# Kernel optimization log

Hardware: AMD Instinct MI355X
Metric: run time of the kernel (lower is better)

The kernel has to match this reference:

```python
import jax, jax.numpy as jnp
import numpy as np

TAU = 1.0
K_ROUTE = 3
EPS = 1e-8


def setup_inputs() -> dict:
    key = jax.random.key(0)
    ks = jax.random.split(key, 8)
    B, T, D_in, H, D_out, L, d_addr = 8, 8192, 1024, 1024, 1024, 12, 64

    def unit_rows(k, L_, d_):
        U = jax.random.normal(k, (L_, d_), dtype=jnp.float32)
        U = U - U.mean(axis=1, keepdims=True)
        return U / (jnp.linalg.norm(U, axis=1, keepdims=True) + EPS)

    def norm_tape(k, shape):
        W = jax.random.normal(k, shape, dtype=jnp.float32)
        # F.normalize over last two dims per expert
        n = jnp.sqrt(jnp.sum(W * W, axis=tuple(range(1, W.ndim)), keepdims=True)) + 1e-12
        return W / n

    x = jax.random.normal(ks[0], (B, T, D_in), dtype=jnp.float32)
    P_w = jax.random.normal(ks[1], (d_addr, D_in), dtype=jnp.float32) / np.sqrt(D_in)
    U1 = unit_rows(ks[2], L, d_addr)
    U2 = unit_rows(ks[3], L, d_addr)
    U3 = unit_rows(ks[4], L, d_addr)
    W1 = norm_tape(ks[5], (L, H, D_in))
    W2 = norm_tape(ks[6], (L, D_out, H))
    b2 = norm_tape(ks[7], (L, D_out))
    return {"x": x, "P_w": P_w, "U1": U1, "U2": U2, "U3": U3,
            "W1": W1, "W2": W2, "b2": b2}


def _route_combine_weights(x_addr, U, k, tau):
    """Top-k routing -> dense combine matrix C: [N, L], zero off the top-k.
    Mathematically identical to scattering softmax(topv/tau) onto expert slots,
    matching RouterTopK.forward + the grouped dispatch/combine."""
    z = x_addr @ U.T                      # [N, L]
    topv, topi = jax.lax.top_k(z, k)      # [N, k]
    w = jax.nn.softmax(topv / (tau + EPS), axis=1)
    N, L = z.shape
    rows = jnp.arange(N)[:, None]
    return jnp.zeros((N, L), z.dtype).at[rows, topi].add(w)


def _mixture(inp, C, W):
    """y[n] = sum_e C[n,e] * (W[e] @ inp[n]); C is top-k sparse per row.
    Loop over the small fixed expert count L (12) with one dense GEMM each;
    equals _apply_mixture_grouped since C is zero for unselected experts."""
    L = W.shape[0]
    y = jnp.zeros((inp.shape[0], W.shape[1]), inp.dtype)
    for e in range(L):
        y = y + C[:, e:e + 1] * (inp @ W[e].T)
    return y


def reference(x, P_w, U1, U2, U3, W1, W2, b2):
    B, T, D = x.shape
    xf = x.reshape(B * T, D)              # [N, D_in]
    xa = xf @ P_w.T                       # [N, d_addr]
    C1 = _route_combine_weights(xa, U1, K_ROUTE, TAU)
    C2 = _route_combine_weights(xa, U2, K_ROUTE, TAU)
    C3 = _route_combine_weights(xa, U3, K_ROUTE, TAU)
    h = jax.nn.gelu(_mixture(xf, C1, W1), approximate=False)  # nn.GELU (exact)
    y = _mixture(h, C2, W2) + C3 @ b2      # routed bias == _apply_bias_grouped
    return y.reshape(B, T, -1)
```

## Files before the change

### kernel.cpp

```cpp
#include <hip/hip_runtime.h>

#define NTOT 65536

typedef __attribute__((ext_vector_type(8))) short bf16x8;
typedef __attribute__((ext_vector_type(4))) float f32x4;

__device__ __forceinline__ float bf2f(unsigned short u) {
    union { unsigned int i; float f; } v; v.i = ((unsigned int)u) << 16; return v.f;
}
__device__ __forceinline__ unsigned short f2bf(float f) {
    union { float f; unsigned int i; } v; v.f = f;
    unsigned int i = v.i;
    return (unsigned short)((i + 0x7FFFu + ((i >> 16) & 1u)) >> 16);
}
__device__ __forceinline__ float lo16(unsigned int v) { return bf2f((unsigned short)(v & 0xFFFFu)); }
__device__ __forceinline__ float hi16(unsigned int v) { return bf2f((unsigned short)(v >> 16)); }

__device__ __forceinline__ void gload16(const unsigned short* g, unsigned short* l) {
    __builtin_amdgcn_global_load_lds((const __attribute__((address_space(1))) void*)(g),
                                     (__attribute__((address_space(3))) void*)(l), 16, 0, 0);
}

__global__ __launch_bounds__(256) void cvt_bf16(const float* __restrict__ src,
                                                unsigned short* __restrict__ dst) {
    size_t i = ((size_t)blockIdx.x * 256 + threadIdx.x) * 8;
    float4 a = *(const float4*)(src + i);
    float4 b = *(const float4*)(src + i + 4);
    unsigned int o0 = (unsigned int)f2bf(a.x) | ((unsigned int)f2bf(a.y) << 16);
    unsigned int o1 = (unsigned int)f2bf(a.z) | ((unsigned int)f2bf(a.w) << 16);
    unsigned int o2 = (unsigned int)f2bf(b.x) | ((unsigned int)f2bf(b.y) << 16);
    unsigned int o3 = (unsigned int)f2bf(b.z) | ((unsigned int)f2bf(b.w) << 16);
    uint4 o = {o0, o1, o2, o3};
    *(uint4*)(dst + i) = o;
}

__global__ void zero_counts(int* c1, int* c2) {
    if (threadIdx.x < 16) { c1[threadIdx.x] = 0; c2[threadIdx.x] = 0; }
}

__global__ __launch_bounds__(256, 2) void addr_xa(const float* __restrict__ X,
                                                  const float* __restrict__ Pw,
                                                  double* __restrict__ xa, int tok_base) {
    __shared__ float xs[64 * 133];
    __shared__ float ps[64 * 133];
    const int tid = threadIdx.x;
    const int tb = blockIdx.x * 64;
    const int ta = tid & 15, tt = tid >> 4;
    double acc[4][4];
    for (int i = 0; i < 4; i++) for (int j = 0; j < 4; j++) acc[i][j] = 0.0;
    for (int kc = 0; kc < 8; ++kc) {
        int k0 = kc * 128;
        for (int i = 0; i < 8; ++i) {
            int lin = i * 256 + tid;
            int row = lin >> 5;
            int c4 = lin & 31;
            float4 v = *(const float4*)&X[(size_t)(tok_base + tb + row) * 1024 + k0 + c4 * 4];
            *(float4*)&xs[row * 133 + c4 * 4] = v;
            float4 w = *(const float4*)&Pw[(size_t)row * 1024 + k0 + c4 * 4];
            *(float4*)&ps[row * 133 + c4 * 4] = w;
        }
        __syncthreads();
        for (int k = 0; k < 128; k += 4) {
            float4 xv[4], pv[4];
            for (int i = 0; i < 4; ++i) xv[i] = *(const float4*)&xs[(tt * 4 + i) * 133 + k];
            for (int j = 0; j < 4; ++j) pv[j] = *(const float4*)&ps[(ta * 4 + j) * 133 + k];
            for (int i = 0; i < 4; ++i)
                for (int j = 0; j < 4; ++j) {
                    double s = acc[i][j];
                    s += (double)xv[i].x * (double)pv[j].x;
                    s += (double)xv[i].y * (double)pv[j].y;
                    s += (double)xv[i].z * (double)pv[j].z;
                    s += (double)xv[i].w * (double)pv[j].w;
                    acc[i][j] = s;
                }
        }
        __syncthreads();
    }
    for (int i = 0; i < 4; ++i)
        for (int j = 0; j < 4; ++j)
            xa[(size_t)(tb + tt * 4 + i) * 64 + ta * 4 + j] = acc[i][j];
}

__global__ __launch_bounds__(256) void route_kernel(
    const double* __restrict__ xa,
    const float* __restrict__ U1, const float* __restrict__ U2, const float* __restrict__ U3,
    int* __restrict__ counts1, int* __restrict__ counts2,
    int* __restrict__ bucket1, float* __restrict__ bucketw1,
    int* __restrict__ bucket2, float* __restrict__ bucketw2,
    int* __restrict__ topi3, float* __restrict__ topw3, int Nc) {
    __shared__ float Us[3 * 12 * 64];
    __shared__ int lcnt1[12], lcnt2[12], gbase1[12], gbase2[12];
    int tid = threadIdx.x;
    for (int i = tid; i < 3 * 12 * 64; i += 256) {
        int l = i / (12 * 64), rem = i % (12 * 64);
        const float* Up = (l == 0 ? U1 : (l == 1 ? U2 : U3));
        Us[i] = Up[rem];
    }
    if (tid < 12) { lcnt1[tid] = 0; lcnt2[tid] = 0; }
    __syncthreads();
    int n = blockIdx.x * 256 + tid;
    double xv[64];
    for (int a = 0; a < 64; a += 2) {
        double2 v = *(const double2*)&xa[(size_t)n * 64 + a];
        xv[a] = v.x; xv[a + 1] = v.y;
    }
    int ei[3][3]; float ew[3][3];
    for (int l = 0; l < 3; l++) {
        double z[12];
        for (int e = 0; e < 12; e++) {
            double s = 0.0;
            const float* u = &Us[(l * 12 + e) * 64];
            for (int a = 0; a < 64; a++) s += xv[a] * (double)u[a];
            z[e] = s;
        }
        int i0 = 0, i1 = 0, i2 = 0; double v0 = -1e300, v1 = -1e300, v2 = -1e300;
        for (int e = 0; e < 12; e++) {
            double v = z[e];
            if (v > v0)      { v2 = v1; i2 = i1; v1 = v0; i1 = i0; v0 = v; i0 = e; }
            else if (v > v1) { v2 = v1; i2 = i1; v1 = v; i1 = e; }
            else if (v > v2) { v2 = v; i2 = e; }
        }
        float inv = 1.0f / (1.0f + 1e-8f);
        float e1 = expf((float)(v1 - v0) * inv), e2 = expf((float)(v2 - v0) * inv);
        float s = 1.0f + e1 + e2;
        ew[l][0] = 1.0f / s; ew[l][1] = e1 / s; ew[l][2] = e2 / s;
        ei[l][0] = i0; ei[l][1] = i1; ei[l][2] = i2;
    }
    int lpos1[3], lpos2[3];
    for (int s = 0; s < 3; s++) {
        lpos1[s] = atomicAdd(&lcnt1[ei[0][s]], 1);
        lpos2[s] = atomicAdd(&lcnt2[ei[1][s]], 1);
    }
    __syncthreads();
    if (tid < 12) {
        gbase1[tid] = atomicAdd(&counts1[tid], lcnt1[tid]);
        gbase2[tid] = atomicAdd(&counts2[tid], lcnt2[tid]);
    }
    __syncthreads();
    for (int s = 0; s < 3; s++) {
        int e = ei[0][s]; int pos = gbase1[e] + lpos1[s];
        bucket1[e * Nc + pos] = (s << 16) | n;
        bucketw1[e * Nc + pos] = ew[0][s];
        e = ei[1][s]; pos = gbase2[e] + lpos2[s];
        bucket2[e * Nc + pos] = (s << 16) | n;
        bucketw2[e * Nc + pos] = ew[1][s];
        topi3[n * 3 + s] = ei[2][s];
        topw3[n * 3 + s] = ew[2][s];
    }
}

__global__ __launch_bounds__(256) void grouped_gemm(
    const unsigned short* __restrict__ A,
    const unsigned short* __restrict__ W,
    const int* __restrict__ bucket, const float* __restrict__ bucketw,
    const int* __restrict__ counts,
    unsigned short* __restrict__ part, int Nc) {
    __shared__ unsigned short As[128 * 32];
    __shared__ unsigned short Bs[128 * 32];
    __shared__ int ids[128];
    __shared__ float wts[128];
    int bx = blockIdx.x;
    int e = -1, mt = 0, accum = 0, Me = 0;
    for (int ee = 0; ee < 12; ee++) {
        int c = counts[ee];
        int t = (c + 127) >> 7;
        if (e < 0 && bx < accum + t) { e = ee; mt = bx - accum; Me = c; }
        accum += t;
    }
    if (e < 0) return;
    int nt = blockIdx.y;
    int tid = threadIdx.x, lane = tid & 63, w = tid >> 6;
    int m0 = mt << 7;
    if (tid < 128) {
        int r = m0 + tid; if (r >= Me) r = Me - 1;
        ids[tid] = bucket[e * Nc + r];
        wts[tid] = bucketw[e * Nc + r];
    }
    __syncthreads();
    int seg = lane & 3;
    int rA0 = w * 16 + (lane >> 2);
    int rA1 = rA0 + 64;
    const unsigned short* a0p = A + (size_t)(ids[rA0] & 0xFFFF) * 1024 + seg * 8;
    const unsigned short* a1p = A + (size_t)(ids[rA1] & 0xFFFF) * 1024 + seg * 8;
    const unsigned short* b0p = W + (size_t)e * 1048576 + (size_t)(nt * 128 + rA0) * 1024 + seg * 8;
    const unsigned short* b1p = W + (size_t)e * 1048576 + (size_t)(nt * 128 + rA1) * 1024 + seg * 8;
    unsigned short* AsL0 = &As[w * 512 + lane * 8];
    unsigned short* AsL1 = &As[(w + 4) * 512 + lane * 8];
    unsigned short* BsL0 = &Bs[w * 512 + lane * 8];
    unsigned short* BsL1 = &Bs[(w + 4) * 512 + lane * 8];
    f32x4 acc[4][4];
    for (int i = 0; i < 4; i++) for (int j = 0; j < 4; j++) acc[i][j] = (f32x4){0.f, 0.f, 0.f, 0.f};
    int wr0 = (w & 1) * 64, wc0 = (w >> 1) * 64;
    for (int it = 0; it < 32; ++it) {
        int k0 = it * 32;
        gload16(a0p + k0, AsL0);
        gload16(a1p + k0, AsL1);
        gload16(b0p + k0, BsL0);
        gload16(b1p + k0, BsL1);
        __syncthreads();
        int q = lane >> 4, l15 = lane & 15;
        bf16x8 af[4], bfr[4];
        for (int i = 0; i < 4; i++) af[i]  = *(const bf16x8*)&As[(wr0 + i * 16 + l15) * 32 + q * 8];
        for (int j = 0; j < 4; j++) bfr[j] = *(const bf16x8*)&Bs[(wc0 + j * 16 + l15) * 32 + q * 8];
        for (int i = 0; i < 4; i++)
            for (int j = 0; j < 4; j++)
                acc[i][j] = __builtin_amdgcn_mfma_f32_16x16x32_bf16(af[i], bfr[j], acc[i][j], 0, 0, 0);
        __syncthreads();
    }
    int q = lane >> 4, l15 = lane & 15;
    for (int i = 0; i < 4; i++) {
        for (int r = 0; r < 4; r++) {
            int row = wr0 + i * 16 + q * 4 + r;
            if (m0 + row >= Me) continue;
            int id = ids[row];
            int n = id & 0xFFFF, slot = id >> 16;
            float wt = wts[row];
            size_t base = ((size_t)slot * Nc + n) * 1024 + (size_t)(nt * 128 + wc0);
            for (int j = 0; j < 4; j++)
                part[base + j * 16 + l15] = f2bf(acc[i][j][r] * wt);
        }
    }
}

__global__ __launch_bounds__(256) void combine_gelu(const unsigned short* __restrict__ part,
                                                    unsigned short* __restrict__ h, int Nc) {
    size_t idx = ((size_t)blockIdx.x * 256 + threadIdx.x) * 8;
    const size_t S = (size_t)Nc * 1024;
    uint4 a = *(const uint4*)(part + idx);
    uint4 b = *(const uint4*)(part + S + idx);
    uint4 c = *(const uint4*)(part + 2 * S + idx);
    unsigned int pa[4] = {a.x, a.y, a.z, a.w};
    unsigned int pb[4] = {b.x, b.y, b.z, b.w};
    unsigned int pc[4] = {c.x, c.y, c.z, c.w};
    unsigned int po[4];
    for (int k = 0; k < 4; k++) {
        float s0 = lo16(pa[k]) + lo16(pb[k]) + lo16(pc[k]);
        float s1 = hi16(pa[k]) + hi16(pb[k]) + hi16(pc[k]);
        float g0 = 0.5f * s0 * (1.0f + erff(s0 * 0.70710678118654752f));
        float g1 = 0.5f * s1 * (1.0f + erff(s1 * 0.70710678118654752f));
        po[k] = (unsigned int)f2bf(g0) | ((unsigned int)f2bf(g1) << 16);
    }
    uint4 o = {po[0], po[1], po[2], po[3]};
    *(uint4*)(h + idx) = o;
}

__global__ __launch_bounds__(256) void final_out(const unsigned short* __restrict__ part,
                                                 const int* __restrict__ topi3,
                                                 const float* __restrict__ topw3,
                                                 const float* __restrict__ b2,
                                                 float* __restrict__ out, int Nc) {
    size_t idx = ((size_t)blockIdx.x * 256 + threadIdx.x) * 8;
    const size_t S = (size_t)Nc * 1024;
    int n = (int)(idx >> 10), col = (int)(idx & 1023);
    uint4 a = *(const uint4*)(part + idx);
    uint4 b = *(const uint4*)(part + S + idx);
    uint4 c = *(const uint4*)(part + 2 * S + idx);
    int e0 = topi3[n * 3 + 0], e1 = topi3[n * 3 + 1], e2 = topi3[n * 3 + 2];
    float w0 = topw3[n * 3 + 0], w1 = topw3[n * 3 + 1], w2 = topw3[n * 3 + 2];
    unsigned int pa[4] = {a.x, a.y, a.z, a.w};
    unsigned int pb[4] = {b.x, b.y, b.z, b.w};
    unsigned int pc[4] = {c.x, c.y, c.z, c.w};
    float r[8];
    for (int k = 0; k < 4; k++) {
        r[2 * k]     = lo16(pa[k]) + lo16(pb[k]) + lo16(pc[k]);
        r[2 * k + 1] = hi16(pa[k]) + hi16(pb[k]) + hi16(pc[k]);
    }
    const float* q0 = b2 + (size_t)e0 * 1024 + col;
    const float* q1 = b2 + (size_t)e1 * 1024 + col;
    const float* q2 = b2 + (size_t)e2 * 1024 + col;
    float4 q0a = *(const float4*)q0, q0b = *(const float4*)(q0 + 4);
    float4 q1a = *(const float4*)q1, q1b = *(const float4*)(q1 + 4);
    float4 q2a = *(const float4*)q2, q2b = *(const float4*)(q2 + 4);
    float bz[8] = {q0a.x * w0 + q1a.x * w1 + q2a.x * w2, q0a.y * w0 + q1a.y * w1 + q2a.y * w2,
                   q0a.z * w0 + q1a.z * w1 + q2a.z * w2, q0a.w * w0 + q1a.w * w1 + q2a.w * w2,
                   q0b.x * w0 + q1b.x * w1 + q2b.x * w2, q0b.y * w0 + q1b.y * w1 + q2b.y * w2,
                   q0b.z * w0 + q1b.z * w1 + q2b.z * w2, q0b.w * w0 + q1b.w * w1 + q2b.w * w2};
    float4 o0 = {r[0] + bz[0], r[1] + bz[1], r[2] + bz[2], r[3] + bz[3]};
    float4 o1 = {r[4] + bz[4], r[5] + bz[5], r[6] + bz[6], r[7] + bz[7]};
    *(float4*)(out + idx) = o0;
    *(float4*)(out + idx + 4) = o1;
}

struct WsPlan {
    size_t w1b, w2b, xb, xa, c1, c2, bk1, bw1, bk2, bw2, ti, tw, h, part, total;
};
static WsPlan plan_ws(size_t Nc) {
    auto al = [](size_t x) { return (x + 255) & ~(size_t)255; };
    WsPlan p; size_t o = 0;
    p.w1b = o; o = al(o + (size_t)12 * 1024 * 1024 * 2);
    p.w2b = o; o = al(o + (size_t)12 * 1024 * 1024 * 2);
    p.xb  = o; o = al(o + Nc * 1024 * 2);
    p.xa  = o; o = al(o + Nc * 64 * 8);
    p.c1  = o; o = al(o + 64);
    p.c2  = o; o = al(o + 64);
    p.bk1 = o; o = al(o + 12 * Nc * 4);
    p.bw1 = o; o = al(o + 12 * Nc * 4);
    p.bk2 = o; o = al(o + 12 * Nc * 4);
    p.bw2 = o; o = al(o + 12 * Nc * 4);
    p.ti  = o; o = al(o + Nc * 3 * 4);
    p.tw  = o; o = al(o + Nc * 3 * 4);
    p.h   = o; o = al(o + Nc * 1024 * 2);
    p.part= o; o = al(o + (size_t)3 * Nc * 1024 * 2);
    p.total = o;
    return p;
}

extern "C" void kernel_launch(void* const* d_in, const int* in_sizes, int n_in,
                              void* d_out, int out_size, void* d_ws, size_t ws_size,
                              hipStream_t stream) {
    const float* X  = (const float*)d_in[0];
    const float* Pw = (const float*)d_in[1];
    const float* U1 = (const float*)d_in[2];
    const float* U2 = (const float*)d_in[3];
    const float* U3 = (const float*)d_in[4];
    const float* W1 = (const float*)d_in[5];
    const float* W2 = (const float*)d_in[6];
    const float* B2 = (const float*)d_in[7];
    float* OUT = (float*)d_out;

    int C = 1;
    while (C < 64 && plan_ws(NTOT / C).total > ws_size) C <<= 1;
    int Nc = NTOT / C;
    WsPlan p = plan_ws((size_t)Nc);

    char* ws = (char*)d_ws;
    unsigned short* W1b  = (unsigned short*)(ws + p.w1b);
    unsigned short* W2b  = (unsigned short*)(ws + p.w2b);
    unsigned short* Xb   = (unsigned short*)(ws + p.xb);
    double* xa      = (double*)(ws + p.xa);
    int* counts1    = (int*)(ws + p.c1);
    int* counts2    = (int*)(ws + p.c2);
    int* bucket1    = (int*)(ws + p.bk1);
    float* bucketw1 = (float*)(ws + p.bw1);
    int* bucket2    = (int*)(ws + p.bk2);
    float* bucketw2 = (float*)(ws + p.bw2);
    int* topi3      = (int*)(ws + p.ti);
    float* topw3    = (float*)(ws + p.tw);
    unsigned short* h    = (unsigned short*)(ws + p.h);
    unsigned short* part = (unsigned short*)(ws + p.part);

    cvt_bf16<<<6144, 256, 0, stream>>>(W1, W1b);
    cvt_bf16<<<6144, 256, 0, stream>>>(W2, W2b);

    int gg_tiles = 3 * Nc / 128 + 12;
    for (int c = 0; c < C; ++c) {
        int base = c * Nc;
        zero_counts<<<1, 64, 0, stream>>>(counts1, counts2);
        cvt_bf16<<<Nc / 2, 256, 0, stream>>>(X + (size_t)base * 1024, Xb);
        addr_xa<<<Nc / 64, 256, 0, stream>>>(X, Pw, xa, base);
        route_kernel<<<Nc / 256, 256, 0, stream>>>(xa, U1, U2, U3, counts1, counts2,
                                                   bucket1, bucketw1, bucket2, bucketw2,
                                                   topi3, topw3, Nc);
        grouped_gemm<<<dim3(gg_tiles, 8), 256, 0, stream>>>(Xb, W1b,
                                                            bucket1, bucketw1, counts1, part, Nc);
        combine_gelu<<<Nc / 2, 256, 0, stream>>>(part, h, Nc);
        grouped_gemm<<<dim3(gg_tiles, 8), 256, 0, stream>>>(h, W2b,
                                                            bucket2, bucketw2, counts2, part, Nc);
        final_out<<<Nc / 2, 256, 0, stream>>>(part, topi3, topw3, B2,
                                              OUT + (size_t)base * 1024, Nc);
    }
}
```

Measured before the change: 2.191 ms.

## Precompose router matrices with address projection into a single fp64 logits GEMM

Precomputes M = U·P_w for all 36 router rows once, so the router logits come directly from X·M^T rather than first forming the 64-dim address vector and then projecting it. The new fp64 z_gemm stages X and M tiles into LDS with direct global-to-LDS loads and an XOR swizzle. The routing kernel then only reads the 36 logits per token. This drops the separate per-token 64x12x3 projection and the xa round trip, but the fp64 GEMM now has 36 output columns instead of 64, and reassociating the sum may change near-tie top-k choices.

```diff
diff --git a/kernel.cpp b/kernel.cpp
--- a/kernel.cpp
+++ b/kernel.cpp
@@ -16,7 +16,7 @@
 __device__ __forceinline__ float lo16(unsigned int v) { return bf2f((unsigned short)(v & 0xFFFFu)); }
 __device__ __forceinline__ float hi16(unsigned int v) { return bf2f((unsigned short)(v >> 16)); }
 
-__device__ __forceinline__ void gload16(const unsigned short* g, unsigned short* l) {
+__device__ __forceinline__ void gload16(const void* g, void* l) {
     __builtin_amdgcn_global_load_lds((const __attribute__((address_space(1))) void*)(g),
                                      (__attribute__((address_space(3))) void*)(l), 16, 0, 0);
 }
@@ -38,84 +38,109 @@
     if (threadIdx.x < 16) { c1[threadIdx.x] = 0; c2[threadIdx.x] = 0; }
 }
 
-__global__ __launch_bounds__(256, 2) void addr_xa(const float* __restrict__ X,
-                                                  const float* __restrict__ Pw,
-                                                  double* __restrict__ xa, int tok_base) {
-    __shared__ float xs[64 * 133];
-    __shared__ float ps[64 * 133];
+__global__ __launch_bounds__(256) void compute_M(const float* __restrict__ U1,
+                                                 const float* __restrict__ U2,
+                                                 const float* __restrict__ U3,
+                                                 const float* __restrict__ Pw,
+                                                 double* __restrict__ M) {
+    int le = blockIdx.x;
+    int l = le / 12, e = le % 12;
+    const float* U = (l == 0 ? U1 : (l == 1 ? U2 : U3)) + e * 64;
+    int c = threadIdx.x * 4;
+    double a0 = 0.0, a1 = 0.0, a2 = 0.0, a3 = 0.0;
+    for (int a = 0; a < 64; a++) {
+        double u = (double)U[a];
+        float4 p = *(const float4*)&Pw[(size_t)a * 1024 + c];
+        a0 += u * (double)p.x; a1 += u * (double)p.y;
+        a2 += u * (double)p.z; a3 += u * (double)p.w;
+    }
+    double* mp = M + (size_t)le * 1024 + c;
+    mp[0] = a0; mp[1] = a1; mp[2] = a2; mp[3] = a3;
+}
+
+__global__ __launch_bounds__(256) void z_gemm(const float* __restrict__ X,
+                                              const double* __restrict__ Mg,
+                                              double* __restrict__ z, int tok_base) {
+    __shared__ __align__(16) float xs[128 * 64];
+    __shared__ __align__(16) double Ms[36 * 64];
     const int tid = threadIdx.x;
-    const int tb = blockIdx.x * 64;
-    const int ta = tid & 15, tt = tid >> 4;
-    double acc[4][4];
-    for (int i = 0; i < 4; i++) for (int j = 0; j < 4; j++) acc[i][j] = 0.0;
-    for (int kc = 0; kc < 8; ++kc) {
-        int k0 = kc * 128;
-        for (int i = 0; i < 8; ++i) {
-            int lin = i * 256 + tid;
-            int row = lin >> 5;
-            int c4 = lin & 31;
-            float4 v = *(const float4*)&X[(size_t)(tok_base + tb + row) * 1024 + k0 + c4 * 4];
-            *(float4*)&xs[row * 133 + c4 * 4] = v;
-            float4 w = *(const float4*)&Pw[(size_t)row * 1024 + k0 + c4 * 4];
-            *(float4*)&ps[row * 133 + c4 * 4] = w;
+    const int w = tid >> 6, lane = tid & 63;
+    const int tok0 = tid & 63, tok1 = tok0 + 64;
+    const int eg = tid >> 6;
+    const int tb = blockIdx.x * 128;
+
+    double acc[2][9];
+#pragma unroll
+    for (int t = 0; t < 2; t++)
+#pragma unroll
+        for (int j = 0; j < 9; j++) acc[t][j] = 0.0;
+
+    for (int kc = 0; kc < 16; ++kc) {
+        int k0 = kc * 64;
+        for (int i = w; i < 50; i += 4) {
+            if (i < 32) {
+                int r = i * 4 + (lane >> 4);
+                int p = lane & 15;
+                const float* g = X + (size_t)(tok_base + tb + r) * 1024 + k0 + ((p ^ (r & 7)) << 2);
+                gload16(g, xs + i * 256 + lane * 4);
+            } else {
+                int ii = i - 32;
+                int e = ii * 2 + (lane >> 5);
+                const double* g = Mg + (size_t)e * 1024 + k0 + ((lane & 31) << 1);
+                gload16(g, Ms + ii * 128 + lane * 2);
+            }
         }
         __syncthreads();
-        for (int k = 0; k < 128; k += 4) {
-            float4 xv[4], pv[4];
-            for (int i = 0; i < 4; ++i) xv[i] = *(const float4*)&xs[(tt * 4 + i) * 133 + k];
-            for (int j = 0; j < 4; ++j) pv[j] = *(const float4*)&ps[(ta * 4 + j) * 133 + k];
-            for (int i = 0; i < 4; ++i)
-                for (int j = 0; j < 4; ++j) {
-                    double s = acc[i][j];
-                    s += (double)xv[i].x * (double)pv[j].x;
-                    s += (double)xv[i].y * (double)pv[j].y;
-                    s += (double)xv[i].z * (double)pv[j].z;
-                    s += (double)xv[i].w * (double)pv[j].w;
-                    acc[i][j] = s;
-                }
+#pragma unroll
+        for (int kq = 0; kq < 16; ++kq) {
+            int p = (kq ^ (tok0 & 7)) << 2;
+            float4 xa4 = *(const float4*)&xs[(tok0 << 6) + p];
+            float4 xb4 = *(const float4*)&xs[(tok1 << 6) + p];
+            double xd00 = (double)xa4.x, xd01 = (double)xa4.y,
+                   xd02 = (double)xa4.z, xd03 = (double)xa4.w;
+            double xd10 = (double)xb4.x, xd11 = (double)xb4.y,
+                   xd12 = (double)xb4.z, xd13 = (double)xb4.w;
+            const double* mp = &Ms[(eg * 9) * 64 + (kq << 2)];
+#pragma unroll
+            for (int j = 0; j < 9; j++) {
+                double2 m0 = *(const double2*)(mp + j * 64);
+                double2 m1 = *(const double2*)(mp + j * 64 + 2);
+                acc[0][j] += xd00 * m0.x + xd01 * m0.y + xd02 * m1.x + xd03 * m1.y;
+                acc[1][j] += xd10 * m0.x + xd11 * m0.y + xd12 * m1.x + xd13 * m1.y;
+            }
         }
         __syncthreads();
     }
-    for (int i = 0; i < 4; ++i)
-        for (int j = 0; j < 4; ++j)
-            xa[(size_t)(tb + tt * 4 + i) * 64 + ta * 4 + j] = acc[i][j];
-}
-
-__global__ __launch_bounds__(256) void route_kernel(
-    const double* __restrict__ xa,
-    const float* __restrict__ U1, const float* __restrict__ U2, const float* __restrict__ U3,
+    double* zp0 = z + (size_t)(tb + tok0) * 36 + eg * 9;
+    double* zp1 = z + (size_t)(tb + tok1) * 36 + eg * 9;
+#pragma unroll
+    for (int j = 0; j < 9; j++) { zp0[j] = acc[0][j]; zp1[j] = acc[1][j]; }
+}
+
+__global__ __launch_bounds__(256) void route2(
+    const double* __restrict__ z,
     int* __restrict__ counts1, int* __restrict__ counts2,
     int* __restrict__ bucket1, float* __restrict__ bucketw1,
     int* __restrict__ bucket2, float* __restrict__ bucketw2,
     int* __restrict__ topi3, float* __restrict__ topw3, int Nc) {
-    __shared__ float Us[3 * 12 * 64];
     __shared__ int lcnt1[12], lcnt2[12], gbase1[12], gbase2[12];
     int tid = threadIdx.x;
-    for (int i = tid; i < 3 * 12 * 64; i += 256) {
-        int l = i / (12 * 64), rem = i % (12 * 64);
-        const float* Up = (l == 0 ? U1 : (l == 1 ? U2 : U3));
-        Us[i] = Up[rem];
-    }
     if (tid < 12) { lcnt1[tid] = 0; lcnt2[tid] = 0; }
     __syncthreads();
     int n = blockIdx.x * 256 + tid;
-    double xv[64];
-    for (int a = 0; a < 64; a += 2) {
-        double2 v = *(const double2*)&xa[(size_t)n * 64 + a];
-        xv[a] = v.x; xv[a + 1] = v.y;
-    }
     int ei[3][3]; float ew[3][3];
     for (int l = 0; l < 3; l++) {
-        double z[12];
+        double zz[12];
+        const double* zp = z + (size_t)n * 36 + l * 12;
+#pragma unroll
+        for (int e = 0; e < 12; e += 2) {
+            double2 v = *(const double2*)(zp + e);
+            zz[e] = v.x; zz[e + 1] = v.y;
+        }
+        int i0 = 0, i1 = 0, i2 = 0; double v0 = -1e300, v1 = -1e300, v2 = -1e300;
+#pragma unroll
         for (int e = 0; e < 12; e++) {
-            double s = 0.0;
-            const float* u = &Us[(l * 12 + e) * 64];
-            for (int a = 0; a < 64; a++) s += xv[a] * (double)u[a];
-            z[e] = s;
-        }
-        int i0 = 0, i1 = 0, i2 = 0; double v0 = -1e300, v1 = -1e300, v2 = -1e300;
-        for (int e = 0; e < 12; e++) {
-            double v = z[e];
+            double v = zz[e];
             if (v > v0)      { v2 = v1; i2 = i1; v1 = v0; i1 = i0; v0 = v; i0 = e; }
             else if (v > v1) { v2 = v1; i2 = i1; v1 = v; i1 = e; }
             else if (v > v2) { v2 = v; i2 = e; }
@@ -282,7 +307,7 @@
 }
 
 struct WsPlan {
-    size_t w1b, w2b, xb, xa, c1, c2, bk1, bw1, bk2, bw2, ti, tw, h, part, total;
+    size_t w1b, w2b, xb, m, z, c1, c2, bk1, bw1, bk2, bw2, ti, tw, h, part, total;
 };
 static WsPlan plan_ws(size_t Nc) {
     auto al = [](size_t x) { return (x + 255) & ~(size_t)255; };
@@ -290,7 +315,8 @@
     p.w1b = o; o = al(o + (size_t)12 * 1024 * 1024 * 2);
     p.w2b = o; o = al(o + (size_t)12 * 1024 * 1024 * 2);
     p.xb  = o; o = al(o + Nc * 1024 * 2);
-    p.xa  = o; o = al(o + Nc * 64 * 8);
+    p.m   = o; o = al(o + (size_t)36 * 1024 * 8);
+    p.z   = o; o = al(o + Nc * 36 * 8);
     p.c1  = o; o = al(o + 64);
     p.c2  = o; o = al(o + 64);
     p.bk1 = o; o = al(o + 12 * Nc * 4);
@@ -327,7 +353,8 @@
     unsigned short* W1b  = (unsigned short*)(ws + p.w1b);
     unsigned short* W2b  = (unsigned short*)(ws + p.w2b);
     unsigned short* Xb   = (unsigned short*)(ws + p.xb);
-    double* xa      = (double*)(ws + p.xa);
+    double* Md      = (double*)(ws + p.m);
+    double* zbuf    = (double*)(ws + p.z);
     int* counts1    = (int*)(ws + p.c1);
     int* counts2    = (int*)(ws + p.c2);
     int* bucket1    = (int*)(ws + p.bk1);
@@ -341,16 +368,17 @@
 
     cvt_bf16<<<6144, 256, 0, stream>>>(W1, W1b);
     cvt_bf16<<<6144, 256, 0, stream>>>(W2, W2b);
+    compute_M<<<36, 256, 0, stream>>>(U1, U2, U3, Pw, Md);
 
     int gg_tiles = 3 * Nc / 128 + 12;
     for (int c = 0; c < C; ++c) {
         int base = c * Nc;
         zero_counts<<<1, 64, 0, stream>>>(counts1, counts2);
         cvt_bf16<<<Nc / 2, 256, 0, stream>>>(X + (size_t)base * 1024, Xb);
-        addr_xa<<<Nc / 64, 256, 0, stream>>>(X, Pw, xa, base);
-        route_kernel<<<Nc / 256, 256, 0, stream>>>(xa, U1, U2, U3, counts1, counts2,
-                                                   bucket1, bucketw1, bucket2, bucketw2,
-                                                   topi3, topw3, Nc);
+        z_gemm<<<Nc / 128, 256, 0, stream>>>(X, Md, zbuf, base);
+        route2<<<Nc / 256, 256, 0, stream>>>(zbuf, counts1, counts2,
+                                             bucket1, bucketw1, bucket2, bucketw2,
+                                             topi3, topw3, Nc);
         grouped_gemm<<<dim3(gg_tiles, 8), 256, 0, stream>>>(Xb, W1b,
                                                             bucket1, bucketw1, counts1, part, Nc);
         combine_gelu<<<Nc / 2, 256, 0, stream>>>(part, h, Nc);
```

Result: faster. 2.075 ms (-5.3%).
